# Performance work log

Measured on AMD Instinct MI355X. Metric: run time of the kernel, lower is better.

Reference implementation:

```python
import jax, jax.numpy as jnp
import numpy as np

B, S, H = 2, 2048, 2048
NH, NKV, HD = 32, 8, 64
G = NH // NKV  # query heads per KV head
SCALE = HD ** -0.5
NEG = -1e9


def setup_inputs() -> dict:
    key = jax.random.key(0)
    ks = jax.random.split(key, 6)
    hidden_states = jax.random.normal(ks[0], (B, S, H), dtype=jnp.float32)
    # causal additive mask, broadcastable over batch and heads
    causal = jnp.tril(jnp.ones((S, S), dtype=bool))
    attention_mask = jnp.where(causal, 0.0, NEG).astype(jnp.float32)[None, None]
    sd = 1.0 / np.sqrt(H)
    wq = jax.random.normal(ks[1], (H, NH * HD), dtype=jnp.float32) * sd
    wk = jax.random.normal(ks[2], (H, NKV * HD), dtype=jnp.float32) * sd
    wv = jax.random.normal(ks[3], (H, NKV * HD), dtype=jnp.float32) * sd
    wo = jax.random.normal(ks[4], (NH * HD, H), dtype=jnp.float32) * sd
    return {"hidden_states": hidden_states, "attention_mask": attention_mask,
            "wq": wq, "wk": wk, "wv": wv, "wo": wo}


def reference(hidden_states, attention_mask, wq, wk, wv, wo):
    b, s, _ = hidden_states.shape
    # projections; group q heads as [b, kv_head, group, s, d] to avoid
    # materializing expanded K/V (same math as expand+matmul)
    q = (hidden_states @ wq).reshape(b, s, NKV, G, HD)
    k = (hidden_states @ wk).reshape(b, s, NKV, HD)
    v = (hidden_states @ wv).reshape(b, s, NKV, HD)
    q = jnp.einsum('bskgd->bkgsd', q)
    k = jnp.einsum('bskd->bksd', k)
    v = jnp.einsum('bskd->bksd', v)
    scores = jnp.einsum('bkgsd,bktd->bkgst', q, k) * SCALE  # [b,kv,G,s,s]
    mask = attention_mask  # [1,1,S,S] broadcastable
    scores = scores + mask[:, :, None] if mask.ndim == 4 else scores + mask
    attn = jax.nn.softmax(scores.astype(jnp.float32), axis=-1).astype(q.dtype)
    out = jnp.einsum('bkgst,bktd->bkgsd', attn, v)
    out = jnp.einsum('bkgsd->bskgd', out).reshape(b, s, NH * HD)
    return out @ wo
```

## Files before the change

kernel.cpp:

```cpp
#include <hip/hip_runtime.h>
#include <hip/hip_bf16.h>
#include <type_traits>


#define B_SZ 2
#define S_LEN 2048
#define HID 2048
#define NHEADS 32
#define NKVH 8
#define HEADD 64
#define QKV_N 3072
#define QK_SCALE 0.18033688f
#define FIXED_M 12.0f

typedef __attribute__((ext_vector_type(8))) short bf16x8;
typedef __attribute__((ext_vector_type(4))) float f32x4;

__device__ __forceinline__ float bf2f(unsigned short u) {
  union { unsigned int i; float f; } v;
  v.i = ((unsigned int)u) << 16;
  return v.f;
}
__device__ __forceinline__ unsigned short f2bf(float f) {
  union { float f; unsigned int i; } v;
  v.f = f;
  unsigned int r = v.i + 0x7fffu + ((v.i >> 16) & 1u);
  return (unsigned short)(r >> 16);
}
#if __has_builtin(__builtin_amdgcn_exp2f)
__device__ __forceinline__ float exp2v(float x) { return __builtin_amdgcn_exp2f(x); }
#else
__device__ __forceinline__ float exp2v(float x) { return exp2f(x); }
#endif
__device__ __forceinline__ void gload_lds16(const unsigned short* g, unsigned short* l) {
  __builtin_amdgcn_global_load_lds(
      (const __attribute__((address_space(1))) unsigned int*)g,
      (__attribute__((address_space(3))) unsigned int*)l, 16, 0, 0);
}
__device__ __forceinline__ int pv_perm(int s) {
  return (((s >> 2) & 7) << 3) | (((s >> 5) & 1) << 2) | (s & 3);
}

__global__ void cvt_bf16_kernel(const float4* __restrict__ in,
                                ushort4* __restrict__ out, int n4) {
  int i = blockIdx.x * blockDim.x + threadIdx.x;
  if (i >= n4) return;
  float4 v = in[i];
  ushort4 o;
  o.x = f2bf(v.x); o.y = f2bf(v.y); o.z = f2bf(v.z); o.w = f2bf(v.w);
  out[i] = o;
}

__global__ void transpose_qkvw_kernel(const float* __restrict__ wq,
                                      const float* __restrict__ wk,
                                      const float* __restrict__ wv,
                                      unsigned short* __restrict__ out) {
  __shared__ float tile[32][33];
  int n0 = blockIdx.x * 32;
  int r0 = blockIdx.y * 32;
  const float* src;
  int C, cb;
  float scale;
  if (n0 < 2048) { src = wq; C = 2048; cb = n0; scale = QK_SCALE; }
  else if (n0 < 2560) { src = wk; C = 512; cb = n0 - 2048; scale = 1.0f; }
  else { src = wv; C = 512; cb = n0 - 2560; scale = 1.0f; }
  int x = threadIdx.x, y = threadIdx.y;
#pragma unroll
  for (int i = 0; i < 32; i += 8)
    tile[y + i][x] = src[(size_t)(r0 + y + i) * C + cb + x];
  __syncthreads();
#pragma unroll
  for (int i = 0; i < 32; i += 8)
    out[(size_t)(n0 + y + i) * HID + r0 + x] = f2bf(tile[x][y + i] * scale);
}

__global__ void transpose_cvt_kernel(const float* __restrict__ in,
                                     unsigned short* __restrict__ out,
                                     int R, int C) {
  __shared__ float tile[32][33];
  int c0 = blockIdx.x * 32, r0 = blockIdx.y * 32;
  int x = threadIdx.x, y = threadIdx.y;
#pragma unroll
  for (int i = 0; i < 32; i += 8)
    tile[y + i][x] = in[(size_t)(r0 + y + i) * C + c0 + x];
  __syncthreads();
#pragma unroll
  for (int i = 0; i < 32; i += 8)
    out[(size_t)(c0 + y + i) * R + r0 + x] = f2bf(tile[x][y + i]);
}

__global__ void transpose_v_kernel(const unsigned short* __restrict__ QKV,
                                   unsigned short* __restrict__ Vt) {
  __shared__ unsigned short tile[32][33];
  int s0 = blockIdx.x * 32, d0 = blockIdx.y * 32;
  int bk = blockIdx.z;
  int b = bk >> 3, kvh = bk & 7;
  int x = threadIdx.x, y = threadIdx.y;
#pragma unroll
  for (int i = 0; i < 32; i += 8)
    tile[y + i][x] =
        QKV[(size_t)(b * S_LEN + s0 + y + i) * QKV_N + 2560 + kvh * HEADD + d0 + x];
  __syncthreads();
  int colg = s0 + x;
  int colp = (colg & ~63) | pv_perm(colg & 63);
#pragma unroll
  for (int i = 0; i < 32; i += 8)
    Vt[((size_t)(b * NKVH + kvh) * HEADD + d0 + y + i) * S_LEN + colp] =
        tile[x][y + i];
}

template <typename OutT>
__global__ __launch_bounds__(512, 2) void gemm256_kernel(
    const unsigned short* __restrict__ A, const unsigned short* __restrict__ Bt,
    OutT* __restrict__ C, int N, int K) {
  extern __shared__ unsigned short sm[];
  const int tid = threadIdx.x;
  const int wave = tid >> 6;
  const int lane = tid & 63;
  const int wm = wave >> 2, wn = wave & 3;
  const int rl = lane & 15, g = lane >> 4;
  const int nwg = gridDim.x;
  const int orig = blockIdx.x;
  const int swz = (orig & 7) * (nwg >> 3) + (orig >> 3);
  const int ntn = N >> 8;
  const int m0 = (swz / ntn) << 8;
  const int n0 = (swz % ntn) << 8;
  f32x4 acc[8][4] = {};

  size_t aoff[2], boff[2];
  int ldst[2];
#pragma unroll
  for (int i = 0; i < 2; ++i) {
    int cc = tid + i * 512;
    int row = cc >> 2, slot = cc & 3;
    int xk = (slot ^ ((row >> 1) & 3)) * 8;
    aoff[i] = (size_t)(m0 + row) * K + xk;
    boff[i] = (size_t)(n0 + row) * K + xk;
    ldst[i] = (wave * 64 + i * 512) * 8;
  }
  const int NT = K >> 6;

#pragma unroll
  for (int i = 0; i < 2; ++i) gload_lds16(A + aoff[i], sm + ldst[i]);
#pragma unroll
  for (int i = 0; i < 2; ++i) gload_lds16(Bt + boff[i], sm + 32768 + ldst[i]);
#pragma unroll
  for (int i = 0; i < 2; ++i) gload_lds16(A + aoff[i] + 32, sm + 8192 + ldst[i]);
#pragma unroll
  for (int i = 0; i < 2; ++i) gload_lds16(Bt + boff[i] + 32, sm + 40960 + ldst[i]);

  int cur = 0;
  for (int t = 0; t < NT; ++t) {
    const int nxt = cur ^ 1;
    const bool st = (t + 1 < NT);
    const size_t k1 = (size_t)(t + 1) << 6;
    unsigned short* An0 = sm + (nxt * 2 + 0) * 8192;
    unsigned short* An1 = sm + (nxt * 2 + 1) * 8192;
    unsigned short* Bn0 = sm + 32768 + (nxt * 2 + 0) * 8192;
    unsigned short* Bn1 = sm + 32768 + (nxt * 2 + 1) * 8192;
    const unsigned short* Ac0 = sm + (cur * 2 + 0) * 8192;
    const unsigned short* Ac1 = sm + (cur * 2 + 1) * 8192;
    const unsigned short* Bc0 = sm + 32768 + (cur * 2 + 0) * 8192;
    const unsigned short* Bc1 = sm + 32768 + (cur * 2 + 1) * 8192;
    bf16x8 bA[4], bB[4];
    if (st) {
      gload_lds16(A + aoff[0] + k1, An0 + ldst[0]);
      gload_lds16(A + aoff[1] + k1, An0 + ldst[1]);
    }
    __builtin_amdgcn_sched_barrier(0);
    if (st) asm volatile("s_waitcnt vmcnt(6)" ::: "memory");
    else    asm volatile("s_waitcnt vmcnt(4)" ::: "memory");
    __builtin_amdgcn_s_barrier();
    __builtin_amdgcn_sched_barrier(0);
#pragma unroll
    for (int nb = 0; nb < 4; ++nb) {
      int rw = wn * 64 + nb * 16 + rl;
      bB[nb] = *(const bf16x8*)&Bc0[rw * 32 + (g ^ ((rw >> 1) & 3)) * 8];
    }
#pragma unroll
    for (int mi = 0; mi < 4; ++mi) {
      int rw = wm * 128 + mi * 16 + rl;
      bA[mi] = *(const bf16x8*)&Ac0[rw * 32 + (g ^ ((rw >> 1) & 3)) * 8];
    }
    __builtin_amdgcn_s_setprio(1);
#pragma unroll
    for (int mi = 0; mi < 4; ++mi)
#pragma unroll
      for (int nb = 0; nb < 4; ++nb)
        acc[mi][nb] = __builtin_amdgcn_mfma_f32_16x16x32_bf16(bA[mi], bB[nb],
                                                              acc[mi][nb], 0, 0, 0);
    __builtin_amdgcn_s_setprio(0);
    if (st) {
      gload_lds16(Bt + boff[0] + k1, Bn0 + ldst[0]);
      gload_lds16(Bt + boff[1] + k1, Bn0 + ldst[1]);
    }
#pragma unroll
    for (int mi = 0; mi < 4; ++mi) {
      int rw = wm * 128 + 64 + mi * 16 + rl;
      bA[mi] = *(const bf16x8*)&Ac0[rw * 32 + (g ^ ((rw >> 1) & 3)) * 8];
    }
    __builtin_amdgcn_s_setprio(1);
#pragma unroll
    for (int mi = 0; mi < 4; ++mi)
#pragma unroll
      for (int nb = 0; nb < 4; ++nb)
        acc[4 + mi][nb] = __builtin_amdgcn_mfma_f32_16x16x32_bf16(bA[mi], bB[nb],
                                                                  acc[4 + mi][nb], 0, 0, 0);
    __builtin_amdgcn_s_setprio(0);
    if (st) {
      gload_lds16(A + aoff[0] + k1 + 32, An1 + ldst[0]);
      gload_lds16(A + aoff[1] + k1 + 32, An1 + ldst[1]);
    }
    __builtin_amdgcn_sched_barrier(0);
    if (st) asm volatile("s_waitcnt vmcnt(6)" ::: "memory");
    else    asm volatile("s_waitcnt vmcnt(0)" ::: "memory");
    __builtin_amdgcn_s_barrier();
    __builtin_amdgcn_sched_barrier(0);
#pragma unroll
    for (int nb = 0; nb < 4; ++nb) {
      int rw = wn * 64 + nb * 16 + rl;
      bB[nb] = *(const bf16x8*)&Bc1[rw * 32 + (g ^ ((rw >> 1) & 3)) * 8];
    }
#pragma unroll
    for (int mi = 0; mi < 4; ++mi) {
      int rw = wm * 128 + mi * 16 + rl;
      bA[mi] = *(const bf16x8*)&Ac1[rw * 32 + (g ^ ((rw >> 1) & 3)) * 8];
    }
    __builtin_amdgcn_s_setprio(1);
#pragma unroll
    for (int mi = 0; mi < 4; ++mi)
#pragma unroll
      for (int nb = 0; nb < 4; ++nb)
        acc[mi][nb] = __builtin_amdgcn_mfma_f32_16x16x32_bf16(bA[mi], bB[nb],
                                                              acc[mi][nb], 0, 0, 0);
    __builtin_amdgcn_s_setprio(0);
    if (st) {
      gload_lds16(Bt + boff[0] + k1 + 32, Bn1 + ldst[0]);
      gload_lds16(Bt + boff[1] + k1 + 32, Bn1 + ldst[1]);
    }
#pragma unroll
    for (int mi = 0; mi < 4; ++mi) {
      int rw = wm * 128 + 64 + mi * 16 + rl;
      bA[mi] = *(const bf16x8*)&Ac1[rw * 32 + (g ^ ((rw >> 1) & 3)) * 8];
    }
    __builtin_amdgcn_s_setprio(1);
#pragma unroll
    for (int mi = 0; mi < 4; ++mi)
#pragma unroll
      for (int nb = 0; nb < 4; ++nb)
        acc[4 + mi][nb] = __builtin_amdgcn_mfma_f32_16x16x32_bf16(bA[mi], bB[nb],
                                                                  acc[4 + mi][nb], 0, 0, 0);
    __builtin_amdgcn_s_setprio(0);
    cur = nxt;
  }
#pragma unroll
  for (int mg = 0; mg < 8; ++mg)
#pragma unroll
    for (int nb = 0; nb < 4; ++nb)
#pragma unroll
      for (int r = 0; r < 4; ++r) {
        int row = m0 + wm * 128 + (mg >> 2) * 64 + (mg & 3) * 16 + g * 4 + r;
        int col = n0 + wn * 64 + nb * 16 + rl;
        float v = acc[mg][nb][r];
        if constexpr (std::is_same_v<OutT, unsigned short>)
          C[(size_t)row * N + col] = f2bf(v);
        else
          C[(size_t)row * N + col] = v;
      }
}

template <typename OutT>
__global__ __launch_bounds__(256) void gemm_bt_kernel(
    const unsigned short* __restrict__ A, const unsigned short* __restrict__ Bt,
    OutT* __restrict__ C, int M, int N, int K) {
  __shared__ unsigned short ldsA[3][128 * 32];
  __shared__ unsigned short ldsB[3][128 * 32];
  const int tid = threadIdx.x;
  const int wave = tid >> 6;
  const int lane = tid & 63;
  const int nwg = gridDim.x;
  const int orig = blockIdx.x;
  const int swz = (orig & 7) * (nwg >> 3) + (orig >> 3);
  const int ntn = N >> 7;
  const int m0 = (swz / ntn) << 7;
  const int n0 = (swz % ntn) << 7;
  const int wr = wave >> 1, wc = wave & 1;
  f32x4 acc[4][4] = {};

  size_t offA[2], offB[2];
#pragma unroll
  for (int i = 0; i < 2; ++i) {
    int cc = tid + i * 256;
    int row = cc >> 2, slot = cc & 3;
    int xk = (slot ^ ((row >> 1) & 3)) * 8;
    offA[i] = (size_t)(m0 + row) * K + xk;
    offB[i] = (size_t)(n0 + row) * K + xk;
  }
  const int rl = lane & 15, g = lane >> 4;
  const int nk = K >> 5;
  const int ldsbase = (wave * 64) * 8;

#pragma unroll
  for (int s = 0; s < 2; ++s) {
#pragma unroll
    for (int i = 0; i < 2; ++i) {
      gload_lds16(A + offA[i] + (s << 5), &ldsA[s][ldsbase + i * 256 * 8]);
      gload_lds16(Bt + offB[i] + (s << 5), &ldsB[s][ldsbase + i * 256 * 8]);
    }
  }
  int cur = 0;

  for (int t = 0; t < nk; ++t) {
    __builtin_amdgcn_sched_barrier(0);
    if (t < nk - 1)
      asm volatile("s_waitcnt vmcnt(4)" ::: "memory");
    else
      asm volatile("s_waitcnt vmcnt(0)" ::: "memory");
    __builtin_amdgcn_s_barrier();
    __builtin_amdgcn_sched_barrier(0);
    if (t + 2 < nk) {
      const int k0 = (t + 2) << 5;
      const int nb = (cur + 2 >= 3) ? cur - 1 : cur + 2;
#pragma unroll
      for (int i = 0; i < 2; ++i) {
        gload_lds16(A + offA[i] + k0, &ldsA[nb][ldsbase + i * 256 * 8]);
        gload_lds16(Bt + offB[i] + k0, &ldsB[nb][ldsbase + i * 256 * 8]);
      }
    }
    const int xs = (g ^ ((rl >> 1) & 3)) * 8;
    bf16x8 a[4], b[4];
#pragma unroll
    for (int mi = 0; mi < 4; ++mi)
      a[mi] = *(const bf16x8*)&ldsA[cur][(wr * 64 + mi * 16 + rl) * 32 + xs];
#pragma unroll
    for (int ni = 0; ni < 4; ++ni)
      b[ni] = *(const bf16x8*)&ldsB[cur][(wc * 64 + ni * 16 + rl) * 32 + xs];
#pragma unroll
    for (int mi = 0; mi < 4; ++mi)
#pragma unroll
      for (int ni = 0; ni < 4; ++ni)
        acc[mi][ni] =
            __builtin_amdgcn_mfma_f32_16x16x32_bf16(a[mi], b[ni], acc[mi][ni], 0, 0, 0);
    cur = (cur + 1 == 3) ? 0 : cur + 1;
  }
#pragma unroll
  for (int mi = 0; mi < 4; ++mi)
#pragma unroll
    for (int ni = 0; ni < 4; ++ni)
#pragma unroll
      for (int r = 0; r < 4; ++r) {
        int row = m0 + wr * 64 + mi * 16 + (lane >> 4) * 4 + r;
        int col = n0 + wc * 64 + ni * 16 + (lane & 15);
        float v = acc[mi][ni][r];
        if constexpr (std::is_same_v<OutT, unsigned short>)
          C[(size_t)row * N + col] = f2bf(v);
        else
          C[(size_t)row * N + col] = v;
      }
}

__global__ __launch_bounds__(256) void mfma_attn_kernel(
    const unsigned short* __restrict__ QKV,
    const unsigned short* __restrict__ Vt,
    unsigned short* __restrict__ O) {
  __shared__ unsigned short Ks[2][64 * 64];
  __shared__ unsigned short Vs[2][64 * 64];
  const int head = blockIdx.y, b = blockIdx.z;
  const int kvh = head >> 2;
  const int tid = threadIdx.x;
  const int w = tid >> 6, lane = tid & 63;
  const int c = lane & 15, g = lane >> 4;
  const int srow = tid >> 3, sslot = tid & 7;
  const int xslot = sslot ^ (srow & 7);

  bf16x8 ones_f;
#pragma unroll
  for (int i = 0; i < 8; ++i) ones_f[i] = (short)0x3F80;

  const unsigned short* Ksrc[2];
  const unsigned short* Vsrc[2];
#pragma unroll
  for (int i = 0; i < 2; ++i) {
    int row = srow + i * 32;
    Ksrc[i] = QKV + (size_t)(b * S_LEN + row) * QKV_N + 2048 + kvh * HEADD + xslot * 8;
    Vsrc[i] = Vt + ((size_t)(b * NKVH + kvh) * HEADD + row) * S_LEN + xslot * 8;
  }

#pragma unroll
  for (int i = 0; i < 2; ++i) {
    gload_lds16(Ksrc[i], &Ks[0][(w * 64 + i * 256) * 8]);
    gload_lds16(Vsrc[i], &Vs[0][(w * 64 + i * 256) * 8]);
  }
  __syncthreads();
  int cur = 0;

  for (int ph = 0; ph < 2; ++ph) {
    const int qt = (ph == 0) ? (int)blockIdx.x : (S_LEN / 64 - 1) - (int)blockIdx.x;
    bf16x8 qf[2];
    {
      const unsigned short* qp =
          QKV + (size_t)(b * S_LEN + qt * 64 + w * 16 + c) * QKV_N + head * HEADD +
          g * 8;
      qf[0] = *(const bf16x8*)(qp);
      qf[1] = *(const bf16x8*)(qp + 32);
    }
    f32x4 o_acc[4] = {};
    f32x4 l_acc = {};

    for (int t = 0; t <= qt; ++t) {
      const int kv0 = t * 64;
      const bool has_next = !(ph == 1 && t == qt);
      if (has_next) {
        const int kvn = (t < qt) ? kv0 + 64 : 0;
        const int nb = cur ^ 1;
#pragma unroll
        for (int i = 0; i < 2; ++i) {
          gload_lds16(Ksrc[i] + (size_t)kvn * QKV_N, &Ks[nb][(w * 64 + i * 256) * 8]);
          gload_lds16(Vsrc[i] + kvn, &Vs[nb][(w * 64 + i * 256) * 8]);
        }
      }
      f32x4 s_acc[4] = {};
      __builtin_amdgcn_s_setprio(1);
#pragma unroll
      for (int ks = 0; ks < 2; ++ks)
#pragma unroll
        for (int kn = 0; kn < 4; ++kn) {
          bf16x8 kf = *(const bf16x8*)&Ks[cur][(kn * 16 + c) * 64 +
                                              (((ks * 4 + g) ^ (c & 7)) * 8)];
          s_acc[kn] =
              __builtin_amdgcn_mfma_f32_16x16x32_bf16(kf, qf[ks], s_acc[kn], 0, 0, 0);
        }
      __builtin_amdgcn_s_setprio(0);
      if (t == qt) {
        const int qg = qt * 64 + w * 16 + c;
#pragma unroll
        for (int kn = 0; kn < 4; ++kn)
#pragma unroll
          for (int r = 0; r < 4; ++r)
            if (kv0 + kn * 16 + g * 4 + r > qg) s_acc[kn][r] = -1e30f;
      }
      float p[4][4];
#pragma unroll
      for (int kn = 0; kn < 4; ++kn)
#pragma unroll
        for (int r = 0; r < 4; ++r)
          p[kn][r] = exp2v(s_acc[kn][r] - FIXED_M);
      union { bf16x8 v; unsigned int w4[4]; } afu[2];
#pragma unroll
      for (int b2 = 0; b2 < 2; ++b2) {
        afu[b2].w4[0] = __builtin_amdgcn_perm(__float_as_uint(p[b2][1]),
                                              __float_as_uint(p[b2][0]), 0x07060302u);
        afu[b2].w4[1] = __builtin_amdgcn_perm(__float_as_uint(p[b2][3]),
                                              __float_as_uint(p[b2][2]), 0x07060302u);
        afu[b2].w4[2] = __builtin_amdgcn_perm(__float_as_uint(p[2 + b2][1]),
                                              __float_as_uint(p[2 + b2][0]), 0x07060302u);
        afu[b2].w4[3] = __builtin_amdgcn_perm(__float_as_uint(p[2 + b2][3]),
                                              __float_as_uint(p[2 + b2][2]), 0x07060302u);
      }
      __builtin_amdgcn_s_setprio(1);
#pragma unroll
      for (int ks2 = 0; ks2 < 2; ++ks2) {
#pragma unroll
        for (int dn = 0; dn < 4; ++dn) {
          bf16x8 vf = *(const bf16x8*)&Vs[cur][(dn * 16 + c) * 64 +
                                              (((ks2 * 4 + g) ^ (c & 7)) * 8)];
          o_acc[dn] =
              __builtin_amdgcn_mfma_f32_16x16x32_bf16(afu[ks2].v, vf, o_acc[dn], 0, 0, 0);
        }
        l_acc = __builtin_amdgcn_mfma_f32_16x16x32_bf16(afu[ks2].v, ones_f, l_acc, 0, 0, 0);
      }
      __builtin_amdgcn_s_setprio(0);
      __syncthreads();
      if (has_next) cur ^= 1;
    }
#pragma unroll
    for (int r = 0; r < 4; ++r) {
      float inv = 1.0f / l_acc[r];
      int row = qt * 64 + w * 16 + g * 4 + r;
#pragma unroll
      for (int dn = 0; dn < 4; ++dn) {
        int col = head * HEADD + dn * 16 + c;
        O[(size_t)(b * S_LEN + row) * (NHEADS * HEADD) + col] =
            f2bf(o_acc[dn][r] * inv);
      }
    }
  }
}

extern "C" void kernel_launch(void* const* d_in, const int* in_sizes, int n_in,
                              void* d_out, int out_size, void* d_ws, size_t ws_size,
                              hipStream_t stream) {
  const float* hs = (const float*)d_in[0];
  const float* wq = (const float*)d_in[2];
  const float* wk = (const float*)d_in[3];
  const float* wv = (const float*)d_in[4];
  const float* wo = (const float*)d_in[5];
  float* out = (float*)d_out;

  hipFuncSetAttribute(reinterpret_cast<const void*>(gemm256_kernel<unsigned short>),
                      hipFuncAttributeMaxDynamicSharedMemorySize, 131072);

  char* ws = (char*)d_ws;
  unsigned short* hs_bf = (unsigned short*)(ws);
  unsigned short* wAllT = (unsigned short*)(ws + ((size_t)16 << 20));
  unsigned short* woT  = (unsigned short*)(ws + ((size_t)28 << 20));
  unsigned short* QKV  = (unsigned short*)(ws + ((size_t)36 << 20));
  unsigned short* Ab   = (unsigned short*)(ws + ((size_t)60 << 20));
  unsigned short* VtB  = (unsigned short*)(ws + ((size_t)76 << 20));

  int n4 = (B_SZ * S_LEN * HID) / 4;
  cvt_bf16_kernel<<<n4 / 256, 256, 0, stream>>>((const float4*)hs, (ushort4*)hs_bf, n4);

  dim3 tb(32, 8);
  transpose_qkvw_kernel<<<dim3(96, 64), tb, 0, stream>>>(wq, wk, wv, wAllT);
  transpose_cvt_kernel<<<dim3(64, 64), tb, 0, stream>>>(wo, woT, NHEADS * HEADD, HID);

  gemm256_kernel<unsigned short><<<192, 512, 131072, stream>>>(
      hs_bf, wAllT, QKV, QKV_N, HID);

  transpose_v_kernel<<<dim3(S_LEN / 32, HEADD / 32, B_SZ * NKVH), tb, 0, stream>>>(
      QKV, VtB);

  mfma_attn_kernel<<<dim3(S_LEN / 128, NHEADS, B_SZ), 256, 0, stream>>>(QKV, VtB, Ab);

  gemm_bt_kernel<float><<<32 * 16, 256, 0, stream>>>(
      Ab, woT, out, B_SZ * S_LEN, HID, HID);
}
```

Measured before the change: 190.0 us.

## Load V fragments directly from global and remap blocks for KV-head locality

```diff
diff --git a/kernel.cpp b/kernel.cpp
--- a/kernel.cpp
+++ b/kernel.cpp
@@ -364,9 +364,13 @@
     const unsigned short* __restrict__ Vt,
     unsigned short* __restrict__ O) {
   __shared__ unsigned short Ks[2][64 * 64];
-  __shared__ unsigned short Vs[2][64 * 64];
-  const int head = blockIdx.y, b = blockIdx.z;
-  const int kvh = head >> 2;
+  const int h = blockIdx.x;
+  const int kvh = h & 7;
+  const int rest = h >> 3;
+  const int b = rest & 1;
+  const int hq = rest >> 1;
+  const int head = kvh * 4 + (hq & 3);
+  const int qpair = hq >> 2;
   const int tid = threadIdx.x;
   const int w = tid >> 6, lane = tid & 63;
   const int c = lane & 15, g = lane >> 4;
@@ -378,24 +382,22 @@
   for (int i = 0; i < 8; ++i) ones_f[i] = (short)0x3F80;
 
   const unsigned short* Ksrc[2];
-  const unsigned short* Vsrc[2];
 #pragma unroll
   for (int i = 0; i < 2; ++i) {
     int row = srow + i * 32;
     Ksrc[i] = QKV + (size_t)(b * S_LEN + row) * QKV_N + 2048 + kvh * HEADD + xslot * 8;
-    Vsrc[i] = Vt + ((size_t)(b * NKVH + kvh) * HEADD + row) * S_LEN + xslot * 8;
-  }
-
-#pragma unroll
-  for (int i = 0; i < 2; ++i) {
+  }
+  const unsigned short* vbase =
+      Vt + ((size_t)(b * NKVH + kvh) * HEADD + c) * S_LEN + g * 8;
+
+#pragma unroll
+  for (int i = 0; i < 2; ++i)
     gload_lds16(Ksrc[i], &Ks[0][(w * 64 + i * 256) * 8]);
-    gload_lds16(Vsrc[i], &Vs[0][(w * 64 + i * 256) * 8]);
-  }
   __syncthreads();
   int cur = 0;
 
   for (int ph = 0; ph < 2; ++ph) {
-    const int qt = (ph == 0) ? (int)blockIdx.x : (S_LEN / 64 - 1) - (int)blockIdx.x;
+    const int qt = (ph == 0) ? qpair : (S_LEN / 64 - 1) - qpair;
     bf16x8 qf[2];
     {
       const unsigned short* qp =
@@ -410,14 +412,19 @@
     for (int t = 0; t <= qt; ++t) {
       const int kv0 = t * 64;
       const bool has_next = !(ph == 1 && t == qt);
+      bf16x8 vf[2][4];
+#pragma unroll
+      for (int ks2 = 0; ks2 < 2; ++ks2)
+#pragma unroll
+        for (int dn = 0; dn < 4; ++dn)
+          vf[ks2][dn] =
+              *(const bf16x8*)(vbase + (size_t)dn * 16 * S_LEN + ks2 * 32 + kv0);
       if (has_next) {
         const int kvn = (t < qt) ? kv0 + 64 : 0;
         const int nb = cur ^ 1;
 #pragma unroll
-        for (int i = 0; i < 2; ++i) {
+        for (int i = 0; i < 2; ++i)
           gload_lds16(Ksrc[i] + (size_t)kvn * QKV_N, &Ks[nb][(w * 64 + i * 256) * 8]);
-          gload_lds16(Vsrc[i] + kvn, &Vs[nb][(w * 64 + i * 256) * 8]);
-        }
       }
       f32x4 s_acc[4] = {};
       __builtin_amdgcn_s_setprio(1);
@@ -461,12 +468,9 @@
 #pragma unroll
       for (int ks2 = 0; ks2 < 2; ++ks2) {
 #pragma unroll
-        for (int dn = 0; dn < 4; ++dn) {
-          bf16x8 vf = *(const bf16x8*)&Vs[cur][(dn * 16 + c) * 64 +
-                                              (((ks2 * 4 + g) ^ (c & 7)) * 8)];
-          o_acc[dn] =
-              __builtin_amdgcn_mfma_f32_16x16x32_bf16(afu[ks2].v, vf, o_acc[dn], 0, 0, 0);
-        }
+        for (int dn = 0; dn < 4; ++dn)
+          o_acc[dn] = __builtin_amdgcn_mfma_f32_16x16x32_bf16(afu[ks2].v, vf[ks2][dn],
+                                                              o_acc[dn], 0, 0, 0);
         l_acc = __builtin_amdgcn_mfma_f32_16x16x32_bf16(afu[ks2].v, ones_f, l_acc, 0, 0, 0);
       }
       __builtin_amdgcn_s_setprio(0);
@@ -521,7 +525,7 @@
   transpose_v_kernel<<<dim3(S_LEN / 32, HEADD / 32, B_SZ * NKVH), tb, 0, stream>>>(
       QKV, VtB);
 
-  mfma_attn_kernel<<<dim3(S_LEN / 128, NHEADS, B_SZ), 256, 0, stream>>>(QKV, VtB, Ab);
+  mfma_attn_kernel<<<1024, 256, 0, stream>>>(QKV, VtB, Ab);
 
   gemm_bt_kernel<float><<<32 * 16, 256, 0, stream>>>(
       Ab, woT, out, B_SZ * S_LEN, HID, HID);
```

Measured after the change: 265.9 us. 39.9% more time.
